# Performance work log

Hardware: AMD Instinct MI355X
Metric: run time of the kernel (lower is better)

## Reference

```python
import jax, jax.numpy as jnp
import numpy as np

N_NODES = 100000
N_EDGES = 1600000
NODE_DIM = 5
HIDDEN = 64
N_LAYERS = 3


def setup_inputs() -> dict:
    key = jax.random.key(0)
    ks = jax.random.split(key, 12)
    s = 0.1
    return {
        "x": jax.random.normal(ks[0], (N_NODES, NODE_DIM), dtype=jnp.float32),
        "edge_index": jax.random.randint(ks[1], (2, N_EDGES), 0, N_NODES, dtype=jnp.int32),
        # message MLP params per layer (stacked over layers)
        "W1": jax.random.normal(ks[2], (N_LAYERS, 2 * NODE_DIM, HIDDEN), dtype=jnp.float32) * s,
        "b1": jnp.zeros((N_LAYERS, HIDDEN), dtype=jnp.float32),
        "W2": jax.random.normal(ks[3], (N_LAYERS, HIDDEN, NODE_DIM), dtype=jnp.float32) * s,
        "b2": jnp.zeros((N_LAYERS, NODE_DIM), dtype=jnp.float32),
        # update MLP params per layer
        "U1": jax.random.normal(ks[4], (N_LAYERS, 2 * NODE_DIM, HIDDEN), dtype=jnp.float32) * s,
        "bu1": jnp.zeros((N_LAYERS, HIDDEN), dtype=jnp.float32),
        "U2": jax.random.normal(ks[5], (N_LAYERS, HIDDEN, NODE_DIM), dtype=jnp.float32) * s,
        "bu2": jnp.zeros((N_LAYERS, NODE_DIM), dtype=jnp.float32),
        # readout
        "Wr": jax.random.normal(ks[6], (NODE_DIM, NODE_DIM), dtype=jnp.float32) * s,
        "br": jnp.zeros((NODE_DIM,), dtype=jnp.float32),
    }


def reference(x, edge_index, W1, b1, W2, b2, U1, bu1, U2, bu2, Wr, br):
    # PyG convention: messages flow from source j = edge_index[0] to target i = edge_index[1]
    src = edge_index[0]
    dst = edge_index[1]
    n = x.shape[0]
    for l in range(N_LAYERS):
        x_i = x[dst]                                   # [E, d] target features
        x_j = x[src]                                   # [E, d] source features
        msg_in = jnp.concatenate([x_i, x_j], axis=-1)  # [E, 2d]
        msg = jax.nn.relu(msg_in @ W1[l] + b1[l]) @ W2[l] + b2[l]   # [E, d]
        aggr = jax.ops.segment_sum(msg, dst, num_segments=n)        # [N, d] scatter-add at targets
        upd_in = jnp.concatenate([x, aggr], axis=-1)   # [N, 2d]
        upd = jax.nn.relu(upd_in @ U1[l] + bu1[l]) @ U2[l] + bu2[l]  # [N, d]
        x = upd + x                                    # residual (in SkeletonGNN.forward)
    return x @ Wr + br
```

## Files before the change

### kernel.cpp

```cpp
#include <hip/hip_runtime.h>

#define N_NODES 100000
#define N_EDGES 1600000
#define DIM 5
#define HID 64
#define N_LAYERS 3
#define SCAN_BLK 256
#define NBLK ((N_NODES + SCAN_BLK - 1) / SCAN_BLK)
#define CNT_STRIDE 16


__global__ __launch_bounds__(256) void hist_kernel(
    const int* __restrict__ ei, int* __restrict__ cnt, int* __restrict__ rank)
{
    int e = blockIdx.x * blockDim.x + threadIdx.x;
    if (e >= N_EDGES) return;
    int dst = ei[N_EDGES + e];
    rank[e] = atomicAdd(&cnt[(long)dst * CNT_STRIDE], 1);
}

__global__ __launch_bounds__(SCAN_BLK) void scan_part_kernel(
    const int* __restrict__ cnt, int* __restrict__ blk_sum)
{
    __shared__ int s[SCAN_BLK];
    int t = threadIdx.x;
    int i = blockIdx.x * SCAN_BLK + t;
    s[t] = (i < N_NODES) ? cnt[(long)i * CNT_STRIDE] : 0;
    __syncthreads();
    for (int off = SCAN_BLK / 2; off > 0; off >>= 1) {
        if (t < off) s[t] += s[t + off];
        __syncthreads();
    }
    if (t == 0) blk_sum[blockIdx.x] = s[0];
}

__global__ __launch_bounds__(512) void scan_blk_kernel(
    const int* __restrict__ blk_sum, int* __restrict__ blk_pref)
{
    __shared__ int s[512];
    int t = threadIdx.x;
    int v = (t < NBLK) ? blk_sum[t] : 0;
    s[t] = v;
    __syncthreads();
    for (int off = 1; off < 512; off <<= 1) {
        int a = (t >= off) ? s[t - off] : 0;
        __syncthreads();
        s[t] += a;
        __syncthreads();
    }
    if (t < NBLK) blk_pref[t] = s[t] - v;
}

__global__ __launch_bounds__(SCAN_BLK) void scan_add_kernel(
    const int* __restrict__ cnt, const int* __restrict__ blk_pref,
    int* __restrict__ row_ptr)
{
    __shared__ int s[SCAN_BLK];
    int t = threadIdx.x;
    int i = blockIdx.x * SCAN_BLK + t;
    int c = (i < N_NODES) ? cnt[(long)i * CNT_STRIDE] : 0;
    s[t] = c;
    __syncthreads();
    for (int off = 1; off < SCAN_BLK; off <<= 1) {
        int a = (t >= off) ? s[t - off] : 0;
        __syncthreads();
        s[t] += a;
        __syncthreads();
    }
    if (i < N_NODES) row_ptr[i] = blk_pref[blockIdx.x] + s[t] - c;
    if (i == 0) row_ptr[N_NODES] = N_EDGES;
}

__global__ __launch_bounds__(256) void scatter_pair_kernel(
    const int* __restrict__ ei, const int* __restrict__ rank,
    const int* __restrict__ row_ptr, int2* __restrict__ spair)
{
    int e = blockIdx.x * blockDim.x + threadIdx.x;
    if (e >= N_EDGES) return;
    int src = ei[e];
    int dst = ei[N_EDGES + e];
    spair[row_ptr[dst] + rank[e]] = make_int2(src, dst);
}


__global__ __launch_bounds__(256) void edge_msg_sorted_kernel(
    const float* __restrict__ x,
    const int2* __restrict__ spair,
    const float* __restrict__ W1, const float* __restrict__ b1,
    const float* __restrict__ W2, const float* __restrict__ b2,
    float* __restrict__ msg_buf)
{
    int e = blockIdx.x * blockDim.x + threadIdx.x;
    if (e >= N_EDGES) return;
    int2 p = spair[e];

    float in[10];
    const float* xi = x + (long)p.y * DIM;
    const float* xj = x + (long)p.x * DIM;
#pragma unroll
    for (int d = 0; d < DIM; ++d) in[d] = xi[d];
#pragma unroll
    for (int d = 0; d < DIM; ++d) in[DIM + d] = xj[d];

    float msg[DIM];
#pragma unroll
    for (int j = 0; j < DIM; ++j) msg[j] = b2[j];

#pragma unroll 8
    for (int h = 0; h < HID; ++h) {
        float acc = b1[h];
#pragma unroll
        for (int d = 0; d < 10; ++d) acc = fmaf(in[d], W1[d * HID + h], acc);
        acc = fmaxf(acc, 0.0f);
#pragma unroll
        for (int j = 0; j < DIM; ++j) msg[j] = fmaf(acc, W2[h * DIM + j], msg[j]);
    }

    float* mp = msg_buf + (long)e * DIM;
#pragma unroll
    for (int j = 0; j < DIM; ++j) mp[j] = msg[j];
}

template <bool FINAL>
__global__ __launch_bounds__(256) void node_gather_update_kernel(
    const float* __restrict__ x,
    const float* __restrict__ msg_buf,
    const int* __restrict__ row_ptr,
    const float* __restrict__ U1, const float* __restrict__ bu1,
    const float* __restrict__ U2, const float* __restrict__ bu2,
    const float* __restrict__ Wr, const float* __restrict__ br,
    float* __restrict__ xout)
{
    int v = blockIdx.x * blockDim.x + threadIdx.x;
    if (v >= N_NODES) return;

    float in[10];
#pragma unroll
    for (int d = 0; d < DIM; ++d) in[d] = x[(long)v * DIM + d];

    float agg[DIM] = {0.f, 0.f, 0.f, 0.f, 0.f};
    int s = row_ptr[v], epos = row_ptr[v + 1];
    for (int e = s; e < epos; ++e) {
        const float* mp = msg_buf + (long)e * DIM;
#pragma unroll
        for (int j = 0; j < DIM; ++j) agg[j] += mp[j];
    }
#pragma unroll
    for (int d = 0; d < DIM; ++d) in[DIM + d] = agg[d];

    float upd[DIM];
#pragma unroll
    for (int j = 0; j < DIM; ++j) upd[j] = bu2[j];

#pragma unroll 8
    for (int h = 0; h < HID; ++h) {
        float acc = bu1[h];
#pragma unroll
        for (int d = 0; d < 10; ++d) acc = fmaf(in[d], U1[d * HID + h], acc);
        acc = fmaxf(acc, 0.0f);
#pragma unroll
        for (int j = 0; j < DIM; ++j) upd[j] = fmaf(acc, U2[h * DIM + j], upd[j]);
    }

    float xn[DIM];
#pragma unroll
    for (int j = 0; j < DIM; ++j) xn[j] = upd[j] + in[j];

    if (FINAL) {
#pragma unroll
        for (int j = 0; j < DIM; ++j) {
            float o = br[j];
#pragma unroll
            for (int d = 0; d < DIM; ++d) o = fmaf(xn[d], Wr[d * DIM + j], o);
            xout[(long)v * DIM + j] = o;
        }
    } else {
#pragma unroll
        for (int j = 0; j < DIM; ++j) xout[(long)v * DIM + j] = xn[j];
    }
}


__global__ __launch_bounds__(256) void edge_msg_kernel(
    const float* __restrict__ x, const int* __restrict__ ei,
    const float* __restrict__ W1, const float* __restrict__ b1,
    const float* __restrict__ W2, const float* __restrict__ b2,
    float* __restrict__ aggr)
{
    int e = blockIdx.x * blockDim.x + threadIdx.x;
    if (e >= N_EDGES) return;
    int src = ei[e];
    int dst = ei[N_EDGES + e];
    float in[10];
    const float* xi = x + (long)dst * DIM;
    const float* xj = x + (long)src * DIM;
#pragma unroll
    for (int d = 0; d < DIM; ++d) in[d] = xi[d];
#pragma unroll
    for (int d = 0; d < DIM; ++d) in[DIM + d] = xj[d];
    float msg[DIM];
#pragma unroll
    for (int j = 0; j < DIM; ++j) msg[j] = b2[j];
#pragma unroll 8
    for (int h = 0; h < HID; ++h) {
        float acc = b1[h];
#pragma unroll
        for (int d = 0; d < 10; ++d) acc = fmaf(in[d], W1[d * HID + h], acc);
        acc = fmaxf(acc, 0.0f);
#pragma unroll
        for (int j = 0; j < DIM; ++j) msg[j] = fmaf(acc, W2[h * DIM + j], msg[j]);
    }
    float* ap = aggr + (long)dst * DIM;
#pragma unroll
    for (int j = 0; j < DIM; ++j) atomicAdd(ap + j, msg[j]);
}

template <bool FINAL>
__global__ __launch_bounds__(256) void node_upd_kernel(
    const float* __restrict__ x, const float* __restrict__ aggr,
    const float* __restrict__ U1, const float* __restrict__ bu1,
    const float* __restrict__ U2, const float* __restrict__ bu2,
    const float* __restrict__ Wr, const float* __restrict__ br,
    float* __restrict__ xout)
{
    int v = blockIdx.x * blockDim.x + threadIdx.x;
    if (v >= N_NODES) return;
    float in[10];
#pragma unroll
    for (int d = 0; d < DIM; ++d) in[d] = x[(long)v * DIM + d];
#pragma unroll
    for (int d = 0; d < DIM; ++d) in[DIM + d] = aggr[(long)v * DIM + d];
    float upd[DIM];
#pragma unroll
    for (int j = 0; j < DIM; ++j) upd[j] = bu2[j];
#pragma unroll 8
    for (int h = 0; h < HID; ++h) {
        float acc = bu1[h];
#pragma unroll
        for (int d = 0; d < 10; ++d) acc = fmaf(in[d], U1[d * HID + h], acc);
        acc = fmaxf(acc, 0.0f);
#pragma unroll
        for (int j = 0; j < DIM; ++j) upd[j] = fmaf(acc, U2[h * DIM + j], upd[j]);
    }
    float xn[DIM];
#pragma unroll
    for (int j = 0; j < DIM; ++j) xn[j] = upd[j] + in[j];
    if (FINAL) {
#pragma unroll
        for (int j = 0; j < DIM; ++j) {
            float o = br[j];
#pragma unroll
            for (int d = 0; d < DIM; ++d) o = fmaf(xn[d], Wr[d * DIM + j], o);
            xout[(long)v * DIM + j] = o;
        }
    } else {
#pragma unroll
        for (int j = 0; j < DIM; ++j) xout[(long)v * DIM + j] = xn[j];
    }
}


static inline size_t alignup(size_t x) { return (x + 255) & ~(size_t)255; }

extern "C" void kernel_launch(void* const* d_in, const int* in_sizes, int n_in,
                              void* d_out, int out_size, void* d_ws, size_t ws_size,
                              hipStream_t stream) {
    const float* x   = (const float*)d_in[0];
    const int*   ei  = (const int*)d_in[1];
    const float* W1  = (const float*)d_in[2];
    const float* b1  = (const float*)d_in[3];
    const float* W2  = (const float*)d_in[4];
    const float* b2  = (const float*)d_in[5];
    const float* U1  = (const float*)d_in[6];
    const float* bu1 = (const float*)d_in[7];
    const float* U2  = (const float*)d_in[8];
    const float* bu2 = (const float*)d_in[9];
    const float* Wr  = (const float*)d_in[10];
    const float* br  = (const float*)d_in[11];
    float* out = (float*)d_out;

    char* ws = (char*)d_ws;

    size_t o_cnt  = 0;
    size_t o_row  = alignup(o_cnt + (size_t)N_NODES * CNT_STRIDE * 4);
    size_t o_bsum = alignup(o_row + (size_t)(N_NODES + 1) * 4);
    size_t o_bpre = alignup(o_bsum + (size_t)NBLK * 4);
    size_t o_sp   = alignup(o_bpre + (size_t)NBLK * 4);
    size_t o_xA   = alignup(o_sp + (size_t)N_EDGES * 8);
    size_t o_xB   = alignup(o_xA + (size_t)N_NODES * DIM * 4);
    size_t o_msg  = alignup(o_xB + (size_t)N_NODES * DIM * 4);
    size_t needed = o_msg + (size_t)N_EDGES * DIM * 4;

    dim3 blk(256);
    dim3 eg((N_EDGES + 255) / 256);
    dim3 ng((N_NODES + 255) / 256);

    if (ws_size < needed) {
        size_t nbytes = (size_t)N_NODES * DIM * sizeof(float);
        float* aggr = (float*)ws;
        float* xA   = (float*)(ws + nbytes);
        float* xB   = (float*)(ws + 2 * nbytes);
        const float* xcur = x;
        for (int l = 0; l < N_LAYERS; ++l) {
            hipMemsetAsync(aggr, 0, nbytes, stream);
            edge_msg_kernel<<<eg, blk, 0, stream>>>(
                xcur, ei, W1 + l * 10 * HID, b1 + l * HID,
                W2 + l * HID * DIM, b2 + l * DIM, aggr);
            if (l < N_LAYERS - 1) {
                float* xn = (l == 0) ? xA : xB;
                node_upd_kernel<false><<<ng, blk, 0, stream>>>(
                    xcur, aggr, U1 + l * 10 * HID, bu1 + l * HID,
                    U2 + l * HID * DIM, bu2 + l * DIM, Wr, br, xn);
                xcur = xn;
            } else {
                node_upd_kernel<true><<<ng, blk, 0, stream>>>(
                    xcur, aggr, U1 + l * 10 * HID, bu1 + l * HID,
                    U2 + l * HID * DIM, bu2 + l * DIM, Wr, br, out);
            }
        }
        return;
    }

    int* cnt      = (int*)(ws + o_cnt);
    int* row_ptr  = (int*)(ws + o_row);
    int* blk_sum  = (int*)(ws + o_bsum);
    int* blk_pref = (int*)(ws + o_bpre);
    int2* spair   = (int2*)(ws + o_sp);
    float* xA     = (float*)(ws + o_xA);
    float* xB     = (float*)(ws + o_xB);
    float* msgbuf = (float*)(ws + o_msg);
    int* rank     = (int*)(ws + o_msg);

    hipMemsetAsync(cnt, 0, (size_t)N_NODES * CNT_STRIDE * 4, stream);
    hist_kernel<<<eg, blk, 0, stream>>>(ei, cnt, rank);
    scan_part_kernel<<<NBLK, SCAN_BLK, 0, stream>>>(cnt, blk_sum);
    scan_blk_kernel<<<1, 512, 0, stream>>>(blk_sum, blk_pref);
    scan_add_kernel<<<NBLK, SCAN_BLK, 0, stream>>>(cnt, blk_pref, row_ptr);
    scatter_pair_kernel<<<eg, blk, 0, stream>>>(ei, rank, row_ptr, spair);

    const float* xcur = x;
    for (int l = 0; l < N_LAYERS; ++l) {
        edge_msg_sorted_kernel<<<eg, blk, 0, stream>>>(
            xcur, spair, W1 + l * 10 * HID, b1 + l * HID,
            W2 + l * HID * DIM, b2 + l * DIM, msgbuf);
        if (l < N_LAYERS - 1) {
            float* xn = (l == 0) ? xA : xB;
            node_gather_update_kernel<false><<<ng, blk, 0, stream>>>(
                xcur, msgbuf, row_ptr, U1 + l * 10 * HID, bu1 + l * HID,
                U2 + l * HID * DIM, bu2 + l * DIM, Wr, br, xn);
            xcur = xn;
        } else {
            node_gather_update_kernel<true><<<ng, blk, 0, stream>>>(
                xcur, msgbuf, row_ptr, U1 + l * 10 * HID, bu1 + l * HID,
                U2 + l * HID * DIM, bu2 + l * DIM, Wr, br, out);
        }
    }
}
```

Measured before the change: 387.3 us.

## Split node gather-update across 8 lanes per node and compact count array

The node gather/update kernel now assigns eight lanes to each node. The lanes split the CSR edge reduction and the 64 hidden units of the update MLP, then combine partial sums with xor shuffles, and lane 0 writes the result. The histogram counter array drops its 16-int padding stride, which shrinks the memset and the scan reads but puts more atomics on shared cache lines. The aim is more parallelism and memory-level concurrency in the gather phase, at the cost of shuffle overhead and idle lanes on low-degree nodes.

```diff
diff --git a/kernel.cpp b/kernel.cpp
--- a/kernel.cpp
+++ b/kernel.cpp
@@ -7,7 +7,6 @@
 #define N_LAYERS 3
 #define SCAN_BLK 256
 #define NBLK ((N_NODES + SCAN_BLK - 1) / SCAN_BLK)
-#define CNT_STRIDE 16
 
 
 __global__ __launch_bounds__(256) void hist_kernel(
@@ -16,7 +15,7 @@
     int e = blockIdx.x * blockDim.x + threadIdx.x;
     if (e >= N_EDGES) return;
     int dst = ei[N_EDGES + e];
-    rank[e] = atomicAdd(&cnt[(long)dst * CNT_STRIDE], 1);
+    rank[e] = atomicAdd(&cnt[dst], 1);
 }
 
 __global__ __launch_bounds__(SCAN_BLK) void scan_part_kernel(
@@ -25,7 +24,7 @@
     __shared__ int s[SCAN_BLK];
     int t = threadIdx.x;
     int i = blockIdx.x * SCAN_BLK + t;
-    s[t] = (i < N_NODES) ? cnt[(long)i * CNT_STRIDE] : 0;
+    s[t] = (i < N_NODES) ? cnt[i] : 0;
     __syncthreads();
     for (int off = SCAN_BLK / 2; off > 0; off >>= 1) {
         if (t < off) s[t] += s[t + off];
@@ -58,7 +57,7 @@
     __shared__ int s[SCAN_BLK];
     int t = threadIdx.x;
     int i = blockIdx.x * SCAN_BLK + t;
-    int c = (i < N_NODES) ? cnt[(long)i * CNT_STRIDE] : 0;
+    int c = (i < N_NODES) ? cnt[i] : 0;
     s[t] = c;
     __syncthreads();
     for (int off = 1; off < SCAN_BLK; off <<= 1) {
@@ -122,7 +121,7 @@
 }
 
 template <bool FINAL>
-__global__ __launch_bounds__(256) void node_gather_update_kernel(
+__global__ __launch_bounds__(256) void gather_update8_kernel(
     const float* __restrict__ x,
     const float* __restrict__ msg_buf,
     const int* __restrict__ row_ptr,
@@ -131,52 +130,64 @@
     const float* __restrict__ Wr, const float* __restrict__ br,
     float* __restrict__ xout)
 {
-    int v = blockIdx.x * blockDim.x + threadIdx.x;
+    int gt = blockIdx.x * blockDim.x + threadIdx.x;
+    int v = gt >> 3;
+    int r = gt & 7;
     if (v >= N_NODES) return;
 
-    float in[10];
-#pragma unroll
-    for (int d = 0; d < DIM; ++d) in[d] = x[(long)v * DIM + d];
+    int s = row_ptr[v], e1 = row_ptr[v + 1];
 
     float agg[DIM] = {0.f, 0.f, 0.f, 0.f, 0.f};
-    int s = row_ptr[v], epos = row_ptr[v + 1];
-    for (int e = s; e < epos; ++e) {
+    for (int e = s + r; e < e1; e += 8) {
         const float* mp = msg_buf + (long)e * DIM;
 #pragma unroll
         for (int j = 0; j < DIM; ++j) agg[j] += mp[j];
     }
 #pragma unroll
-    for (int d = 0; d < DIM; ++d) in[DIM + d] = agg[d];
-
-    float upd[DIM];
-#pragma unroll
-    for (int j = 0; j < DIM; ++j) upd[j] = bu2[j];
-
-#pragma unroll 8
-    for (int h = 0; h < HID; ++h) {
+    for (int m = 1; m < 8; m <<= 1) {
+#pragma unroll
+        for (int j = 0; j < DIM; ++j) agg[j] += __shfl_xor(agg[j], m, 64);
+    }
+
+    float in2[10];
+#pragma unroll
+    for (int d = 0; d < DIM; ++d) in2[d] = x[(long)v * DIM + d];
+#pragma unroll
+    for (int d = 0; d < DIM; ++d) in2[DIM + d] = agg[d];
+
+    float upd[DIM] = {0.f, 0.f, 0.f, 0.f, 0.f};
+#pragma unroll
+    for (int hh = 0; hh < 8; ++hh) {
+        int h = r + hh * 8;
         float acc = bu1[h];
 #pragma unroll
-        for (int d = 0; d < 10; ++d) acc = fmaf(in[d], U1[d * HID + h], acc);
+        for (int d = 0; d < 10; ++d) acc = fmaf(in2[d], U1[d * HID + h], acc);
         acc = fmaxf(acc, 0.0f);
 #pragma unroll
         for (int j = 0; j < DIM; ++j) upd[j] = fmaf(acc, U2[h * DIM + j], upd[j]);
     }
-
-    float xn[DIM];
-#pragma unroll
-    for (int j = 0; j < DIM; ++j) xn[j] = upd[j] + in[j];
-
-    if (FINAL) {
-#pragma unroll
-        for (int j = 0; j < DIM; ++j) {
-            float o = br[j];
-#pragma unroll
-            for (int d = 0; d < DIM; ++d) o = fmaf(xn[d], Wr[d * DIM + j], o);
-            xout[(long)v * DIM + j] = o;
+#pragma unroll
+    for (int m = 1; m < 8; m <<= 1) {
+#pragma unroll
+        for (int j = 0; j < DIM; ++j) upd[j] += __shfl_xor(upd[j], m, 64);
+    }
+
+    if (r == 0) {
+        float xn[DIM];
+#pragma unroll
+        for (int j = 0; j < DIM; ++j) xn[j] = upd[j] + bu2[j] + in2[j];
+        if (FINAL) {
+#pragma unroll
+            for (int j = 0; j < DIM; ++j) {
+                float o = br[j];
+#pragma unroll
+                for (int d = 0; d < DIM; ++d) o = fmaf(xn[d], Wr[d * DIM + j], o);
+                xout[(long)v * DIM + j] = o;
+            }
+        } else {
+#pragma unroll
+            for (int j = 0; j < DIM; ++j) xout[(long)v * DIM + j] = xn[j];
         }
-    } else {
-#pragma unroll
-        for (int j = 0; j < DIM; ++j) xout[(long)v * DIM + j] = xn[j];
     }
 }
 
@@ -282,7 +293,7 @@
     char* ws = (char*)d_ws;
 
     size_t o_cnt  = 0;
-    size_t o_row  = alignup(o_cnt + (size_t)N_NODES * CNT_STRIDE * 4);
+    size_t o_row  = alignup(o_cnt + (size_t)N_NODES * 4);
     size_t o_bsum = alignup(o_row + (size_t)(N_NODES + 1) * 4);
     size_t o_bpre = alignup(o_bsum + (size_t)NBLK * 4);
     size_t o_sp   = alignup(o_bpre + (size_t)NBLK * 4);
@@ -294,6 +305,7 @@
     dim3 blk(256);
     dim3 eg((N_EDGES + 255) / 256);
     dim3 ng((N_NODES + 255) / 256);
+    dim3 ng8((N_NODES * 8 + 255) / 256);
 
     if (ws_size < needed) {
         size_t nbytes = (size_t)N_NODES * DIM * sizeof(float);
@@ -331,7 +343,7 @@
     float* msgbuf = (float*)(ws + o_msg);
     int* rank     = (int*)(ws + o_msg);
 
-    hipMemsetAsync(cnt, 0, (size_t)N_NODES * CNT_STRIDE * 4, stream);
+    hipMemsetAsync(cnt, 0, (size_t)N_NODES * 4, stream);
     hist_kernel<<<eg, blk, 0, stream>>>(ei, cnt, rank);
     scan_part_kernel<<<NBLK, SCAN_BLK, 0, stream>>>(cnt, blk_sum);
     scan_blk_kernel<<<1, 512, 0, stream>>>(blk_sum, blk_pref);
@@ -345,12 +357,12 @@
             W2 + l * HID * DIM, b2 + l * DIM, msgbuf);
         if (l < N_LAYERS - 1) {
             float* xn = (l == 0) ? xA : xB;
-            node_gather_update_kernel<false><<<ng, blk, 0, stream>>>(
+            gather_update8_kernel<false><<<ng8, blk, 0, stream>>>(
                 xcur, msgbuf, row_ptr, U1 + l * 10 * HID, bu1 + l * HID,
                 U2 + l * HID * DIM, bu2 + l * DIM, Wr, br, xn);
             xcur = xn;
         } else {
-            node_gather_update_kernel<true><<<ng, blk, 0, stream>>>(
+            gather_update8_kernel<true><<<ng8, blk, 0, stream>>>(
                 xcur, msgbuf, row_ptr, U1 + l * 10 * HID, bu1 + l * HID,
                 U2 + l * HID * DIM, bu2 + l * DIM, Wr, br, out);
         }
```

Result: no change. 386.1 us (-0.3%).
